# Kernel tuning notes

Hardware: AMD Instinct MI355X
Metric: run time of the kernel (lower is better)

## Reference

```python
import jax, jax.numpy as jnp
import numpy as np

B, NB, K, C, CM, POS = 8, 1024, 9, 32, 128, 2
SIGMA = 0.5
NEG_SLOPE = 0.01  # nn.LeakyReLU default
BN_EPS = 1e-5


def _leaky(x):
    return jnp.where(x >= 0, x, NEG_SLOPE * x)


def _batchnorm(x, gamma, beta):
    # BatchNorm1d, training-mode batch statistics over the point dimension
    mu = jnp.mean(x, axis=0)
    var = jnp.mean((x - mu) ** 2, axis=0)
    return gamma * (x - mu) * jax.lax.rsqrt(var + BN_EPS) + beta


def setup_inputs() -> dict:
    key = jax.random.key(0)
    ks = jax.random.split(key, 8)
    N = B * NB
    positions = jax.random.normal(ks[0], (N, POS), jnp.float32)
    weights = jax.random.normal(ks[1], (N, C), jnp.float32)
    batch = jnp.full((B,), NB, dtype=jnp.int32)  # uniform point counts per graph
    # KernelConv params: kernel_init='grid' -> 3x3 grid of offsets spanning +-sigma
    g = jnp.linspace(-SIGMA, SIGMA, 3, dtype=jnp.float32)
    kernel_positions = jnp.stack(jnp.meshgrid(g, g, indexing='ij'), axis=-1).reshape(K, POS)
    kernel_weights = (jax.random.normal(ks[2], (K, C, C), jnp.float32) / np.float32(np.sqrt(C * K)))
    conv_norm_gamma = jnp.ones((C,), jnp.float32)
    conv_norm_beta = jnp.zeros((C,), jnp.float32)
    # PyG MLP([C, CM, C+POS], act_first=True, plain_last=True)
    W1 = jax.random.normal(ks[3], (C, CM), jnp.float32) / np.float32(np.sqrt(C))
    b1 = jnp.zeros((CM,), jnp.float32)
    bn_gamma = jnp.ones((CM,), jnp.float32)
    bn_beta = jnp.zeros((CM,), jnp.float32)
    W2 = jax.random.normal(ks[4], (CM, C + POS), jnp.float32) / np.float32(np.sqrt(CM))
    b2 = jnp.zeros((C + POS,), jnp.float32)
    return dict(positions=positions, weights=weights, batch=batch,
                kernel_positions=kernel_positions, kernel_weights=kernel_weights,
                conv_norm_gamma=conv_norm_gamma, conv_norm_beta=conv_norm_beta,
                W1=W1, b1=b1, bn_gamma=bn_gamma, bn_beta=bn_beta, W2=W2, b2=b2)


def reference(positions, weights, batch, kernel_positions, kernel_weights,
              conv_norm_gamma, conv_norm_beta, W1, b1, bn_gamma, bn_beta, W2, b2):
    N = positions.shape[0]
    # --- KernelConv: each point spawns K components at pos + kernel offset ---
    conv_pos = (positions[:, None, :] + kernel_positions[None, :, :])  # [N,K,2]
    conv_w = jnp.einsum('nc,kcd->nkd', weights, kernel_weights)        # [N,K,C]
    conv_pos = conv_pos.reshape(B, NB * K, POS)
    conv_w = conv_w.reshape(B, NB * K, C)
    # --- KernelSample: evaluate Gaussian mixture at original positions ---
    p = positions.reshape(B, NB, POS)
    d2 = (jnp.sum(p * p, -1)[:, :, None]
          + jnp.sum(conv_pos * conv_pos, -1)[:, None, :]
          - 2.0 * jnp.einsum('bnd,bmd->bnm', p, conv_pos))             # [B,NB,NB*K]
    Kmat = jnp.exp(-d2 / (2.0 * SIGMA * SIGMA))
    sampled = jnp.einsum('bnm,bmc->bnc', Kmat, conv_w).reshape(N, C)
    x = _leaky(sampled)                                                 # KernelSample nonlinearity
    # conv_norm + residual add of input weights
    x = _batchnorm(x, conv_norm_gamma, conv_norm_beta) + weights
    # MLP: lin -> act -> batchnorm (act_first) -> plain last lin
    h = _batchnorm(_leaky(x @ W1 + b1), bn_gamma, bn_beta)
    mlp_out = h @ W2 + b2                                               # [N, POS + C]
    delta_pos, delta_w = mlp_out[:, :POS], mlp_out[:, POS:]
    return positions + delta_pos, x + delta_w
```

## Files before the change

kernel.cpp:

```cpp
#include <hip/hip_runtime.h>
#include <hip/hip_bf16.h>

#define BB    8
#define NBB   1024
#define KK    9
#define CC    32
#define CMM   128
#define NTOT  (BB*NBB)
#define MM    (NBB*KK)
#define MS    16
#define MR    (MM/MS)
#define NEG   0.01f
#define EPS   1e-5f
#define L2C   (-2.8853900817779268f)

#define OFF_CWT   0
#define SZ_CWT    (BB*CC*MM/2)
#define OFF_CFX   (OFF_CWT + SZ_CWT)
#define OFF_CFY   (OFF_CFX + BB*MM)
#define OFF_CF0   (OFF_CFY + BB*MM)
#define OFF_PART  (OFF_CF0 + BB*MM)
#define SZ_ONE    (NTOT*CC)
#define SZ_PART   (MS*SZ_ONE)
#define OFF_X0    (OFF_PART)
#define OFF_X     (OFF_PART + SZ_ONE)
#define OFF_H0    (OFF_PART + 2*SZ_ONE)
#define OFF_ST    (OFF_PART + SZ_PART)

typedef __attribute__((ext_vector_type(8))) short short8;
typedef __attribute__((ext_vector_type(4))) float f32x4;
typedef __attribute__((ext_vector_type(2))) float f32x2;

static __device__ __forceinline__ unsigned short f2bf_rne(float f) {
    __hip_bfloat16 h = __float2bfloat16(f);
    return *reinterpret_cast<unsigned short*>(&h);
}

__global__ __launch_bounds__(256) void k_convw(const float* __restrict__ pos,
                                               const float* __restrict__ kpos,
                                               const float* __restrict__ w,
                                               const float* __restrict__ kw,
                                               float* __restrict__ cfx,
                                               float* __restrict__ cfy,
                                               float* __restrict__ cf0,
                                               float* __restrict__ stats,
                                               short* __restrict__ cwT) {
    __shared__ unsigned short tile[4*32*144];
    __shared__ unsigned short kwl[KK*CC*CC];
    int t = threadIdx.x;
    int l = t & 63, wv = t >> 6;
    int lane15 = l & 15, quad = l >> 4;
    int blk = blockIdx.x;
    int b = blk >> 4, nbl = blk & 15;
    int n = b*NBB + nbl*64 + wv*16 + lane15;

    if (blk == 0 && t < 320) stats[t] = 0.f;
    #pragma unroll
    for (int rep = 0; rep < 3; ++rep) {
        int gid = blk*256 + t + rep*32768;
        if (gid < BB*MM) {
            int bb = gid / MM;
            int m = gid - bb*MM;
            int np = m / 9, k9 = m - np*9;
            float qx = pos[((size_t)(bb*NBB + np))*2 + 0] + kpos[k9*2 + 0];
            float qy = pos[((size_t)(bb*NBB + np))*2 + 1] + kpos[k9*2 + 1];
            cfx[gid] = -2.f*L2C*qx;
            cfy[gid] = -2.f*L2C*qy;
            cf0[gid] = L2C*(qx*qx + qy*qy);
        }
    }

    for (int u = t; u < KK*CC*CC/4; u += 256) {
        int flat = u*4;
        int row  = flat >> 5;
        int c0   = flat & 31;
        int kk = row >> 5, cp = row & 31;
        f32x4 v = *(const f32x4*)&kw[flat];
        kwl[(kk*CC + c0+0)*CC + cp] = f2bf_rne(v.x);
        kwl[(kk*CC + c0+1)*CC + cp] = f2bf_rne(v.y);
        kwl[(kk*CC + c0+2)*CC + cp] = f2bf_rne(v.z);
        kwl[(kk*CC + c0+3)*CC + cp] = f2bf_rne(v.w);
    }

    f32x4 w0 = *(const f32x4*)&w[(size_t)n*CC + quad*8];
    f32x4 w1 = *(const f32x4*)&w[(size_t)n*CC + quad*8 + 4];
    union { unsigned short us[8]; short8 s; } bfr;
    bfr.us[0] = f2bf_rne(w0.x); bfr.us[1] = f2bf_rne(w0.y);
    bfr.us[2] = f2bf_rne(w0.z); bfr.us[3] = f2bf_rne(w0.w);
    bfr.us[4] = f2bf_rne(w1.x); bfr.us[5] = f2bf_rne(w1.y);
    bfr.us[6] = f2bf_rne(w1.z); bfr.us[7] = f2bf_rne(w1.w);

    __syncthreads();

    f32x4 acc[KK][2];
    #pragma unroll
    for (int kk = 0; kk < KK; ++kk) {
        #pragma unroll
        for (int ct = 0; ct < 2; ++ct) {
            int c = ct*16 + lane15;
            short8 afr = *(const short8*)&kwl[(kk*CC + c)*CC + quad*8];
            acc[kk][ct] = __builtin_amdgcn_mfma_f32_16x16x32_bf16(
                afr, bfr.s, (f32x4)0.f, 0, 0, 0);
        }
    }
    unsigned short* tw = tile + wv*4608;
    #pragma unroll
    for (int kk = 0; kk < KK; ++kk)
        #pragma unroll
        for (int ct = 0; ct < 2; ++ct)
            #pragma unroll
            for (int reg = 0; reg < 4; ++reg) {
                int c = ct*16 + quad*4 + reg;
                tw[c*144 + lane15*9 + kk] = f2bf_rne(acc[kk][ct][reg]);
            }
    __syncthreads();
    short* dst = cwT + (size_t)b*CC*MM + (size_t)(nbl*64 + wv*16)*9;
    #pragma unroll
    for (int it = 0; it < 9; ++it) {
        int u = it*64 + l;
        int c = u / 18, seg = u - c*18;
        short8 v = *(const short8*)&tw[c*144 + seg*8];
        *(short8*)&dst[(size_t)c*MM + seg*8] = v;
    }
}

__global__ __launch_bounds__(256) void k_sample(const float* __restrict__ pos,
                                                const float* __restrict__ cfx,
                                                const float* __restrict__ cfy,
                                                const float* __restrict__ cf0,
                                                const short* __restrict__ cwT,
                                                float* __restrict__ part) {
    int t = threadIdx.x;
    int l = t & 63, w = t >> 6;
    int blk = blockIdx.x;
    int ks = blk & 15, nb = (blk >> 4) & 7, b = blk >> 7;
    int lane15 = l & 15, quad = l >> 4;
    int nbase = b*NBB + nb*128 + w*32;

    float px[2], py[2], cn[2];
    #pragma unroll
    for (int nt = 0; nt < 2; ++nt) {
        int n = nbase + nt*16 + lane15;
        float x = pos[(size_t)n*2], y = pos[(size_t)n*2 + 1];
        px[nt] = x; py[nt] = y; cn[nt] = L2C*(x*x + y*y);
    }
    f32x4 acc[2][2];
    #pragma unroll
    for (int nt = 0; nt < 2; ++nt) { acc[nt][0] = (f32x4)0.f; acc[nt][1] = (f32x4)0.f; }

    const float* bx = cfx + (size_t)b*MM;
    const float* by = cfy + (size_t)b*MM;
    const float* b0 = cf0 + (size_t)b*MM;
    const short* ca0 = cwT + (size_t)b*CC*MM + (size_t)lane15*MM;
    const short* ca1 = ca0 + (size_t)16*MM;

    int m0 = ks*MR + quad*8;
    #pragma unroll 2
    for (int kk = 0; kk < MR/32; ++kk, m0 += 32) {
        short8 a0 = *(const short8*)&ca0[m0];
        short8 a1 = *(const short8*)&ca1[m0];
        f32x4 vx0 = *(const f32x4*)&bx[m0];
        f32x4 vx1 = *(const f32x4*)&bx[m0 + 4];
        f32x4 vy0 = *(const f32x4*)&by[m0];
        f32x4 vy1 = *(const f32x4*)&by[m0 + 4];
        f32x4 v00 = *(const f32x4*)&b0[m0];
        f32x4 v01 = *(const f32x4*)&b0[m0 + 4];
        #pragma unroll
        for (int nt = 0; nt < 2; ++nt) {
            f32x2 Xv = {px[nt], px[nt]};
            f32x2 Yv = {py[nt], py[nt]};
            f32x2 Cv = {cn[nt], cn[nt]};
            f32x2 t0 = (f32x2){v00.x, v00.y} + Cv;
            t0 = (f32x2){vy0.x, vy0.y}*Yv + t0;
            t0 = (f32x2){vx0.x, vx0.y}*Xv + t0;
            f32x2 t1 = (f32x2){v00.z, v00.w} + Cv;
            t1 = (f32x2){vy0.z, vy0.w}*Yv + t1;
            t1 = (f32x2){vx0.z, vx0.w}*Xv + t1;
            f32x2 t2 = (f32x2){v01.x, v01.y} + Cv;
            t2 = (f32x2){vy1.x, vy1.y}*Yv + t2;
            t2 = (f32x2){vx1.x, vx1.y}*Xv + t2;
            f32x2 t3 = (f32x2){v01.z, v01.w} + Cv;
            t3 = (f32x2){vy1.z, vy1.w}*Yv + t3;
            t3 = (f32x2){vx1.z, vx1.w}*Xv + t3;
            float e0 = __builtin_amdgcn_exp2f(t0.x);
            float e1 = __builtin_amdgcn_exp2f(t0.y);
            float e2 = __builtin_amdgcn_exp2f(t1.x);
            float e3 = __builtin_amdgcn_exp2f(t1.y);
            float e4 = __builtin_amdgcn_exp2f(t2.x);
            float e5 = __builtin_amdgcn_exp2f(t2.y);
            float e6 = __builtin_amdgcn_exp2f(t3.x);
            float e7 = __builtin_amdgcn_exp2f(t3.y);
            union { unsigned int u[4]; short8 s; } bf;
            bf.u[0] = (__float_as_uint(e0) >> 16) | (__float_as_uint(e1) & 0xffff0000u);
            bf.u[1] = (__float_as_uint(e2) >> 16) | (__float_as_uint(e3) & 0xffff0000u);
            bf.u[2] = (__float_as_uint(e4) >> 16) | (__float_as_uint(e5) & 0xffff0000u);
            bf.u[3] = (__float_as_uint(e6) >> 16) | (__float_as_uint(e7) & 0xffff0000u);
            acc[nt][0] = __builtin_amdgcn_mfma_f32_16x16x32_bf16(a0, bf.s, acc[nt][0], 0, 0, 0);
            acc[nt][1] = __builtin_amdgcn_mfma_f32_16x16x32_bf16(a1, bf.s, acc[nt][1], 0, 0, 0);
        }
    }
    #pragma unroll
    for (int nt = 0; nt < 2; ++nt) {
        int n = nbase + nt*16 + lane15;
        #pragma unroll
        for (int ct = 0; ct < 2; ++ct) {
            int c = ct*16 + quad*4;
            *(f32x4*)&part[((size_t)ks*NTOT + n)*CC + c] = acc[nt][ct];
        }
    }
}

__global__ __launch_bounds__(256) void k_leaky_stats(const float* __restrict__ part,
                                                     float* __restrict__ x0,
                                                     float* __restrict__ s1) {
    __shared__ float ss[32], sq[32];
    int t = threadIdx.x;
    if (t < 32) { ss[t] = 0.f; sq[t] = 0.f; }
    __syncthreads();
    float lsum = 0.f, lsq = 0.f;
    int base = blockIdx.x * 1024;
    for (int j = 0; j < 4; ++j) {
        int idx = base + j*256 + t;
        float v = 0.f;
        #pragma unroll
        for (int s = 0; s < MS; ++s) v += part[(size_t)s*SZ_ONE + idx];
        v = v >= 0.f ? v : NEG*v;
        x0[idx] = v;
        lsum += v; lsq = fmaf(v, v, lsq);
    }
    atomicAdd(&ss[t & 31], lsum);
    atomicAdd(&sq[t & 31], lsq);
    __syncthreads();
    if (t < 32) { atomicAdd(&s1[t], ss[t]); atomicAdd(&s1[32+t], sq[t]); }
}

__global__ __launch_bounds__(256) void k_mlp1(const float* __restrict__ x0,
                                              const float* __restrict__ wts,
                                              const float* __restrict__ gma,
                                              const float* __restrict__ bta,
                                              const float* __restrict__ W1,
                                              const float* __restrict__ b1,
                                              const float* __restrict__ s1,
                                              float* __restrict__ x,
                                              float* __restrict__ h0,
                                              float* __restrict__ s2) {
    __shared__ float tile[64*68];
    int t = threadIdx.x;
    int l = t & 63, w = t >> 6;
    int blk = blockIdx.x;
    int nb = blk >> 1, jh = blk & 1;
    int n = nb*64 + l;
    int j0 = jh*64 + w*16;

    float xv[32];
    #pragma unroll
    for (int c = 0; c < 32; ++c) {
        float mu  = s1[c] * (1.f/NTOT);
        float var = s1[32+c]*(1.f/NTOT) - mu*mu;
        float a   = gma[c] * rsqrtf(var + EPS);
        float v   = x0[(size_t)n*CC + c];
        xv[c] = a*(v - mu) + bta[c] + wts[(size_t)n*CC + c];
    }
    if (jh == 0 && w == 0) {
        #pragma unroll
        for (int c = 0; c < 32; c += 4)
            *(float4*)&x[(size_t)n*CC + c] = make_float4(xv[c], xv[c+1], xv[c+2], xv[c+3]);
    }
    float acc[16];
    #pragma unroll
    for (int jj = 0; jj < 16; ++jj) acc[jj] = b1[j0 + jj];
    #pragma unroll 4
    for (int c = 0; c < 32; ++c) {
        float xc = xv[c];
        const float* w1r = W1 + c*CMM + j0;
        #pragma unroll
        for (int jj = 0; jj < 16; ++jj)
            acc[jj] = fmaf(xc, w1r[jj], acc[jj]);
    }
    float* hd = h0 + (size_t)n*CMM + j0;
    #pragma unroll
    for (int jj = 0; jj < 16; ++jj) {
        acc[jj] = acc[jj] >= 0.f ? acc[jj] : NEG*acc[jj];
        tile[(w*16 + jj)*68 + l] = acc[jj];
    }
    #pragma unroll
    for (int jj = 0; jj < 16; jj += 4)
        *(float4*)&hd[jj] = make_float4(acc[jj], acc[jj+1], acc[jj+2], acc[jj+3]);
    __syncthreads();
    int jl = t >> 2, grp = t & 3;
    float lsum = 0.f, lsq = 0.f;
    #pragma unroll
    for (int q = 0; q < 4; ++q) {
        f32x4 v = *(const f32x4*)&tile[jl*68 + grp*16 + q*4];
        lsum += v.x + v.y + v.z + v.w;
        lsq = fmaf(v.x, v.x, fmaf(v.y, v.y, fmaf(v.z, v.z, fmaf(v.w, v.w, lsq))));
    }
    lsum += __shfl_xor(lsum, 1); lsq += __shfl_xor(lsq, 1);
    lsum += __shfl_xor(lsum, 2); lsq += __shfl_xor(lsq, 2);
    if (grp == 0) {
        int jg = jh*64 + jl;
        atomicAdd(&s2[jg], lsum);
        atomicAdd(&s2[CMM + jg], lsq);
    }
}

__global__ __launch_bounds__(256) void k_mlp2(const float* __restrict__ h0,
                                              const float* __restrict__ x,
                                              const float* __restrict__ pos,
                                              const float* __restrict__ g2,
                                              const float* __restrict__ bt2,
                                              const float* __restrict__ W2,
                                              const float* __restrict__ b2,
                                              const float* __restrict__ s2,
                                              float* __restrict__ out) {
    __shared__ float red[8][32][35];
    int t = threadIdx.x;
    int lane = t & 63, w = t >> 6;
    int half = lane >> 5;
    int nl = lane & 31;
    int n = blockIdx.x*32 + nl;
    int j0 = w*32 + half*16;
    float hv[16];
    #pragma unroll
    for (int q = 0; q < 4; ++q)
        *(float4*)&hv[q*4] = *(const float4*)&h0[(size_t)n*CMM + j0 + q*4];
    #pragma unroll
    for (int jj = 0; jj < 16; ++jj) {
        int j = j0 + jj;
        float mu  = s2[j] * (1.f/NTOT);
        float var = s2[CMM+j]*(1.f/NTOT) - mu*mu;
        float a   = g2[j] * rsqrtf(var + EPS);
        hv[jj] = a*(hv[jj] - mu) + bt2[j];
    }
    float acc[34];
    #pragma unroll
    for (int c = 0; c < 34; ++c) acc[c] = 0.f;
    for (int jj = 0; jj < 16; ++jj) {
        float h = hv[jj];
        const float* w2r = W2 + (size_t)(j0 + jj)*34;
        #pragma unroll
        for (int c = 0; c < 34; ++c)
            acc[c] = fmaf(h, w2r[c], acc[c]);
    }
    int rid = w*2 + half;
    #pragma unroll
    for (int c = 0; c < 34; ++c) red[rid][nl][c] = acc[c];
    __syncthreads();
    for (int u = t; u < 32*34; u += 256) {
        int r = u / 34, c = u - r*34;
        float v = red[0][r][c] + red[1][r][c] + red[2][r][c] + red[3][r][c]
                + red[4][r][c] + red[5][r][c] + red[6][r][c] + red[7][r][c] + b2[c];
        int nn = blockIdx.x*32 + r;
        if (c < 2)
            out[(size_t)nn*2 + c] = pos[(size_t)nn*2 + c] + v;
        else
            out[16384 + (size_t)nn*32 + (c-2)] = x[(size_t)nn*32 + (c-2)] + v;
    }
}

extern "C" void kernel_launch(void* const* d_in, const int* in_sizes, int n_in,
                              void* d_out, int out_size, void* d_ws, size_t ws_size,
                              hipStream_t stream) {
    const float* positions = (const float*)d_in[0];
    const float* weights   = (const float*)d_in[1];
    const float* kpos = (const float*)d_in[3];
    const float* kw   = (const float*)d_in[4];
    const float* cg   = (const float*)d_in[5];
    const float* cb   = (const float*)d_in[6];
    const float* W1   = (const float*)d_in[7];
    const float* b1   = (const float*)d_in[8];
    const float* bg   = (const float*)d_in[9];
    const float* bb   = (const float*)d_in[10];
    const float* W2   = (const float*)d_in[11];
    const float* b2   = (const float*)d_in[12];
    float* ws  = (float*)d_ws;
    float* out = (float*)d_out;

    float* s1 = ws + OFF_ST;
    float* s2 = ws + OFF_ST + 64;

    k_convw<<<128, 256, 0, stream>>>(positions, kpos, weights, kw,
                                     ws + OFF_CFX, ws + OFF_CFY, ws + OFF_CF0,
                                     s1, (short*)(ws + OFF_CWT));
    k_sample<<<1024, 256, 0, stream>>>(positions, ws + OFF_CFX, ws + OFF_CFY,
                                       ws + OFF_CF0, (const short*)(ws + OFF_CWT),
                                       ws + OFF_PART);
    k_leaky_stats<<<256, 256, 0, stream>>>(ws + OFF_PART, ws + OFF_X0, s1);
    k_mlp1<<<256, 256, 0, stream>>>(ws + OFF_X0, weights, cg, cb, W1, b1,
                                    s1, ws + OFF_X, ws + OFF_H0, s2);
    k_mlp2<<<256, 256, 0, stream>>>(ws + OFF_H0, ws + OFF_X, positions,
                                    bg, bb, W2, b2, s2, out);
}
```

Before: 159.2 us.

## Fuse all stages into one persistent kernel with grid barriers

Replaces the five kernel launches with one 256-block kernel that uses software grid barriers between stages (conv weights, Gaussian sampling, batchnorm stats, MLP). Intermediates stay in shared memory rather than round-tripping through global partial buffers, and the split-M partial reduction is now done inside a block instead of through a separate pass. The goal is to remove launch gaps and global traffic. In exchange, only 256 blocks (one per 32 points) do the heavy sampling loop, which lowers parallelism compared with the previous 1024-block launch. The spin barrier also relies on every block being co-resident on the device.

```diff
diff --git a/kernel.cpp b/kernel.cpp
--- a/kernel.cpp
+++ b/kernel.cpp
@@ -8,24 +8,17 @@
 #define CMM   128
 #define NTOT  (BB*NBB)
 #define MM    (NBB*KK)
-#define MS    16
-#define MR    (MM/MS)
 #define NEG   0.01f
 #define EPS   1e-5f
 #define L2C   (-2.8853900817779268f)
+#define NBLK  256
 
 #define OFF_CWT   0
 #define SZ_CWT    (BB*CC*MM/2)
 #define OFF_CFX   (OFF_CWT + SZ_CWT)
 #define OFF_CFY   (OFF_CFX + BB*MM)
 #define OFF_CF0   (OFF_CFY + BB*MM)
-#define OFF_PART  (OFF_CF0 + BB*MM)
-#define SZ_ONE    (NTOT*CC)
-#define SZ_PART   (MS*SZ_ONE)
-#define OFF_X0    (OFF_PART)
-#define OFF_X     (OFF_PART + SZ_ONE)
-#define OFF_H0    (OFF_PART + 2*SZ_ONE)
-#define OFF_ST    (OFF_PART + SZ_PART)
+#define OFF_ST    (OFF_CF0 + BB*MM)
 
 typedef __attribute__((ext_vector_type(8))) short short8;
 typedef __attribute__((ext_vector_type(4))) float f32x4;
@@ -36,28 +29,59 @@
     return *reinterpret_cast<unsigned short*>(&h);
 }
 
-__global__ __launch_bounds__(256) void k_convw(const float* __restrict__ pos,
-                                               const float* __restrict__ kpos,
-                                               const float* __restrict__ w,
-                                               const float* __restrict__ kw,
-                                               float* __restrict__ cfx,
-                                               float* __restrict__ cfy,
-                                               float* __restrict__ cf0,
-                                               float* __restrict__ stats,
-                                               short* __restrict__ cwT) {
-    __shared__ unsigned short tile[4*32*144];
-    __shared__ unsigned short kwl[KK*CC*CC];
-    int t = threadIdx.x;
-    int l = t & 63, wv = t >> 6;
-    int lane15 = l & 15, quad = l >> 4;
-    int blk = blockIdx.x;
-    int b = blk >> 4, nbl = blk & 15;
-    int n = b*NBB + nbl*64 + wv*16 + lane15;
-
-    if (blk == 0 && t < 320) stats[t] = 0.f;
+__device__ unsigned g_cnt[4];
+__device__ unsigned g_gen[4];
+
+static __device__ __forceinline__ void grid_sync(int i) {
+    __threadfence();
+    __syncthreads();
+    if (threadIdx.x == 0) {
+        unsigned g = __hip_atomic_load(&g_gen[i], __ATOMIC_RELAXED, __HIP_MEMORY_SCOPE_AGENT);
+        unsigned a = __hip_atomic_fetch_add(&g_cnt[i], 1u, __ATOMIC_ACQ_REL, __HIP_MEMORY_SCOPE_AGENT);
+        if (a == NBLK - 1u) {
+            __hip_atomic_store(&g_cnt[i], 0u, __ATOMIC_RELAXED, __HIP_MEMORY_SCOPE_AGENT);
+            __hip_atomic_store(&g_gen[i], g + 1u, __ATOMIC_RELEASE, __HIP_MEMORY_SCOPE_AGENT);
+        } else {
+            while (__hip_atomic_load(&g_gen[i], __ATOMIC_ACQUIRE, __HIP_MEMORY_SCOPE_AGENT) == g)
+                __builtin_amdgcn_s_sleep(2);
+        }
+    }
+    __syncthreads();
+    __threadfence();
+}
+
+#define L_H0   0
+#define L_X    4224
+#define L_X0   5376
+#define L_SCR  6528
+#define L_TOT  15744
+
+__global__ __launch_bounds__(256) void k_fused(
+    const float* __restrict__ pos, const float* __restrict__ wts,
+    const float* __restrict__ kpos, const float* __restrict__ kw,
+    const float* __restrict__ cg, const float* __restrict__ cb,
+    const float* __restrict__ W1, const float* __restrict__ b1,
+    const float* __restrict__ g2, const float* __restrict__ bt2,
+    const float* __restrict__ W2, const float* __restrict__ b2,
+    float* __restrict__ ws, float* __restrict__ out)
+{
+    __shared__ float smem[L_TOT];
+    float* cfx = ws + OFF_CFX;
+    float* cfy = ws + OFF_CFY;
+    float* cf0 = ws + OFF_CF0;
+    float* stats = ws + OFF_ST;
+    short* cwT = (short*)(ws + OFF_CWT);
+
+    const int t = threadIdx.x;
+    const int blk = blockIdx.x;
+    const int l = t & 63, wv = t >> 6;
+    const int lane15 = l & 15, quad = l >> 4;
+    const int b = blk >> 5;
+
+    if (blk == 0) { stats[t] = 0.f; if (t < 64) stats[256 + t] = 0.f; }
     #pragma unroll
-    for (int rep = 0; rep < 3; ++rep) {
-        int gid = blk*256 + t + rep*32768;
+    for (int rep = 0; rep < 2; ++rep) {
+        int gid = rep*65536 + blk*256 + t;
         if (gid < BB*MM) {
             int bb = gid / MM;
             int m = gid - bb*MM;
@@ -69,292 +93,287 @@
             cf0[gid] = L2C*(qx*qx + qy*qy);
         }
     }
-
-    for (int u = t; u < KK*CC*CC/4; u += 256) {
-        int flat = u*4;
-        int row  = flat >> 5;
-        int c0   = flat & 31;
-        int kk = row >> 5, cp = row & 31;
-        f32x4 v = *(const f32x4*)&kw[flat];
-        kwl[(kk*CC + c0+0)*CC + cp] = f2bf_rne(v.x);
-        kwl[(kk*CC + c0+1)*CC + cp] = f2bf_rne(v.y);
-        kwl[(kk*CC + c0+2)*CC + cp] = f2bf_rne(v.z);
-        kwl[(kk*CC + c0+3)*CC + cp] = f2bf_rne(v.w);
-    }
-
-    f32x4 w0 = *(const f32x4*)&w[(size_t)n*CC + quad*8];
-    f32x4 w1 = *(const f32x4*)&w[(size_t)n*CC + quad*8 + 4];
-    union { unsigned short us[8]; short8 s; } bfr;
-    bfr.us[0] = f2bf_rne(w0.x); bfr.us[1] = f2bf_rne(w0.y);
-    bfr.us[2] = f2bf_rne(w0.z); bfr.us[3] = f2bf_rne(w0.w);
-    bfr.us[4] = f2bf_rne(w1.x); bfr.us[5] = f2bf_rne(w1.y);
-    bfr.us[6] = f2bf_rne(w1.z); bfr.us[7] = f2bf_rne(w1.w);
-
-    __syncthreads();
-
-    f32x4 acc[KK][2];
-    #pragma unroll
-    for (int kk = 0; kk < KK; ++kk) {
-        #pragma unroll
-        for (int ct = 0; ct < 2; ++ct) {
-            int c = ct*16 + lane15;
-            short8 afr = *(const short8*)&kwl[(kk*CC + c)*CC + quad*8];
-            acc[kk][ct] = __builtin_amdgcn_mfma_f32_16x16x32_bf16(
-                afr, bfr.s, (f32x4)0.f, 0, 0, 0);
-        }
-    }
-    unsigned short* tw = tile + wv*4608;
-    #pragma unroll
-    for (int kk = 0; kk < KK; ++kk)
-        #pragma unroll
-        for (int ct = 0; ct < 2; ++ct)
-            #pragma unroll
-            for (int reg = 0; reg < 4; ++reg) {
-                int c = ct*16 + quad*4 + reg;
-                tw[c*144 + lane15*9 + kk] = f2bf_rne(acc[kk][ct][reg]);
-            }
-    __syncthreads();
-    short* dst = cwT + (size_t)b*CC*MM + (size_t)(nbl*64 + wv*16)*9;
-    #pragma unroll
-    for (int it = 0; it < 9; ++it) {
-        int u = it*64 + l;
-        int c = u / 18, seg = u - c*18;
-        short8 v = *(const short8*)&tw[c*144 + seg*8];
-        *(short8*)&dst[(size_t)c*MM + seg*8] = v;
-    }
-}
-
-__global__ __launch_bounds__(256) void k_sample(const float* __restrict__ pos,
-                                                const float* __restrict__ cfx,
-                                                const float* __restrict__ cfy,
-                                                const float* __restrict__ cf0,
-                                                const short* __restrict__ cwT,
-                                                float* __restrict__ part) {
-    int t = threadIdx.x;
-    int l = t & 63, w = t >> 6;
-    int blk = blockIdx.x;
-    int ks = blk & 15, nb = (blk >> 4) & 7, b = blk >> 7;
-    int lane15 = l & 15, quad = l >> 4;
-    int nbase = b*NBB + nb*128 + w*32;
-
-    float px[2], py[2], cn[2];
-    #pragma unroll
-    for (int nt = 0; nt < 2; ++nt) {
-        int n = nbase + nt*16 + lane15;
-        float x = pos[(size_t)n*2], y = pos[(size_t)n*2 + 1];
-        px[nt] = x; py[nt] = y; cn[nt] = L2C*(x*x + y*y);
-    }
-    f32x4 acc[2][2];
-    #pragma unroll
-    for (int nt = 0; nt < 2; ++nt) { acc[nt][0] = (f32x4)0.f; acc[nt][1] = (f32x4)0.f; }
-
-    const float* bx = cfx + (size_t)b*MM;
-    const float* by = cfy + (size_t)b*MM;
-    const float* b0 = cf0 + (size_t)b*MM;
-    const short* ca0 = cwT + (size_t)b*CC*MM + (size_t)lane15*MM;
-    const short* ca1 = ca0 + (size_t)16*MM;
-
-    int m0 = ks*MR + quad*8;
-    #pragma unroll 2
-    for (int kk = 0; kk < MR/32; ++kk, m0 += 32) {
+    {
+        unsigned short* kwl  = (unsigned short*)(smem + L_SCR);
+        unsigned short* tile = (unsigned short*)(smem + L_SCR) + 9216;
+        for (int u = t; u < KK*CC*CC/4; u += 256) {
+            int flat = u*4;
+            int row = flat >> 5;
+            int c0 = flat & 31;
+            int kk = row >> 5, cp = row & 31;
+            f32x4 v = *(const f32x4*)&kw[flat];
+            kwl[(kk*CC + c0+0)*CC + cp] = f2bf_rne(v.x);
+            kwl[(kk*CC + c0+1)*CC + cp] = f2bf_rne(v.y);
+            kwl[(kk*CC + c0+2)*CC + cp] = f2bf_rne(v.z);
+            kwl[(kk*CC + c0+3)*CC + cp] = f2bf_rne(v.w);
+        }
+        int nb_ = blk*32 + (wv & 1)*16 + lane15;
+        f32x4 w0 = *(const f32x4*)&wts[(size_t)nb_*CC + quad*8];
+        f32x4 w1v = *(const f32x4*)&wts[(size_t)nb_*CC + quad*8 + 4];
+        union { unsigned short us[8]; short8 s; } bfr;
+        bfr.us[0] = f2bf_rne(w0.x);  bfr.us[1] = f2bf_rne(w0.y);
+        bfr.us[2] = f2bf_rne(w0.z);  bfr.us[3] = f2bf_rne(w0.w);
+        bfr.us[4] = f2bf_rne(w1v.x); bfr.us[5] = f2bf_rne(w1v.y);
+        bfr.us[6] = f2bf_rne(w1v.z); bfr.us[7] = f2bf_rne(w1v.w);
+        __syncthreads();
+        if (wv < 2) {
+            f32x4 acc[KK][2];
+            #pragma unroll
+            for (int kk = 0; kk < KK; ++kk)
+                #pragma unroll
+                for (int ct = 0; ct < 2; ++ct) {
+                    int c = ct*16 + lane15;
+                    short8 afr = *(const short8*)&kwl[(kk*CC + c)*CC + quad*8];
+                    acc[kk][ct] = __builtin_amdgcn_mfma_f32_16x16x32_bf16(
+                        afr, bfr.s, (f32x4)0.f, 0, 0, 0);
+                }
+            unsigned short* tw = tile + wv*4608;
+            #pragma unroll
+            for (int kk = 0; kk < KK; ++kk)
+                #pragma unroll
+                for (int ct = 0; ct < 2; ++ct)
+                    #pragma unroll
+                    for (int reg = 0; reg < 4; ++reg) {
+                        int c = ct*16 + quad*4 + reg;
+                        tw[c*144 + lane15*9 + kk] = f2bf_rne(acc[kk][ct][reg]);
+                    }
+        }
+        __syncthreads();
+        short* dst = cwT + (size_t)b*CC*MM + (size_t)(blk & 31)*288;
+        #pragma unroll
+        for (int it = 0; it < 5; ++it) {
+            int u = it*256 + t;
+            if (u < 1152) {
+                int c = u / 36, seg = u - c*36;
+                const unsigned short* src = tile + (seg < 18 ? 0 : 4608)
+                                          + c*144 + (seg < 18 ? seg : seg - 18)*8;
+                short8 v = *(const short8*)src;
+                *(short8*)&dst[(size_t)c*MM + seg*8] = v;
+            }
+        }
+    }
+    grid_sync(0);
+
+    {
+        const float* bx = cfx + (size_t)b*MM;
+        const float* by = cfy + (size_t)b*MM;
+        const float* b0 = cf0 + (size_t)b*MM;
+        const short* ca0 = cwT + (size_t)b*CC*MM + (size_t)lane15*MM;
+        const short* ca1 = ca0 + (size_t)16*MM;
+
+        float px[2], py[2], cn[2];
+        #pragma unroll
+        for (int nt = 0; nt < 2; ++nt) {
+            int n = blk*32 + nt*16 + lane15;
+            float x = pos[(size_t)n*2], y = pos[(size_t)n*2 + 1];
+            px[nt] = x; py[nt] = y; cn[nt] = L2C*(x*x + y*y);
+        }
+        f32x4 acc[2][2];
+        acc[0][0] = (f32x4)0.f; acc[0][1] = (f32x4)0.f;
+        acc[1][0] = (f32x4)0.f; acc[1][1] = (f32x4)0.f;
+
+        int m0 = wv*2304 + quad*8;
         short8 a0 = *(const short8*)&ca0[m0];
         short8 a1 = *(const short8*)&ca1[m0];
-        f32x4 vx0 = *(const f32x4*)&bx[m0];
-        f32x4 vx1 = *(const f32x4*)&bx[m0 + 4];
-        f32x4 vy0 = *(const f32x4*)&by[m0];
-        f32x4 vy1 = *(const f32x4*)&by[m0 + 4];
-        f32x4 v00 = *(const f32x4*)&b0[m0];
-        f32x4 v01 = *(const f32x4*)&b0[m0 + 4];
-        #pragma unroll
-        for (int nt = 0; nt < 2; ++nt) {
-            f32x2 Xv = {px[nt], px[nt]};
-            f32x2 Yv = {py[nt], py[nt]};
-            f32x2 Cv = {cn[nt], cn[nt]};
-            f32x2 t0 = (f32x2){v00.x, v00.y} + Cv;
-            t0 = (f32x2){vy0.x, vy0.y}*Yv + t0;
-            t0 = (f32x2){vx0.x, vx0.y}*Xv + t0;
-            f32x2 t1 = (f32x2){v00.z, v00.w} + Cv;
-            t1 = (f32x2){vy0.z, vy0.w}*Yv + t1;
-            t1 = (f32x2){vx0.z, vx0.w}*Xv + t1;
-            f32x2 t2 = (f32x2){v01.x, v01.y} + Cv;
-            t2 = (f32x2){vy1.x, vy1.y}*Yv + t2;
-            t2 = (f32x2){vx1.x, vx1.y}*Xv + t2;
-            f32x2 t3 = (f32x2){v01.z, v01.w} + Cv;
-            t3 = (f32x2){vy1.z, vy1.w}*Yv + t3;
-            t3 = (f32x2){vx1.z, vx1.w}*Xv + t3;
-            float e0 = __builtin_amdgcn_exp2f(t0.x);
-            float e1 = __builtin_amdgcn_exp2f(t0.y);
-            float e2 = __builtin_amdgcn_exp2f(t1.x);
-            float e3 = __builtin_amdgcn_exp2f(t1.y);
-            float e4 = __builtin_amdgcn_exp2f(t2.x);
-            float e5 = __builtin_amdgcn_exp2f(t2.y);
-            float e6 = __builtin_amdgcn_exp2f(t3.x);
-            float e7 = __builtin_amdgcn_exp2f(t3.y);
-            union { unsigned int u[4]; short8 s; } bf;
-            bf.u[0] = (__float_as_uint(e0) >> 16) | (__float_as_uint(e1) & 0xffff0000u);
-            bf.u[1] = (__float_as_uint(e2) >> 16) | (__float_as_uint(e3) & 0xffff0000u);
-            bf.u[2] = (__float_as_uint(e4) >> 16) | (__float_as_uint(e5) & 0xffff0000u);
-            bf.u[3] = (__float_as_uint(e6) >> 16) | (__float_as_uint(e7) & 0xffff0000u);
-            acc[nt][0] = __builtin_amdgcn_mfma_f32_16x16x32_bf16(a0, bf.s, acc[nt][0], 0, 0, 0);
-            acc[nt][1] = __builtin_amdgcn_mfma_f32_16x16x32_bf16(a1, bf.s, acc[nt][1], 0, 0, 0);
-        }
-    }
-    #pragma unroll
-    for (int nt = 0; nt < 2; ++nt) {
-        int n = nbase + nt*16 + lane15;
-        #pragma unroll
-        for (int ct = 0; ct < 2; ++ct) {
-            int c = ct*16 + quad*4;
-            *(f32x4*)&part[((size_t)ks*NTOT + n)*CC + c] = acc[nt][ct];
-        }
-    }
-}
-
-__global__ __launch_bounds__(256) void k_leaky_stats(const float* __restrict__ part,
-                                                     float* __restrict__ x0,
-                                                     float* __restrict__ s1) {
-    __shared__ float ss[32], sq[32];
-    int t = threadIdx.x;
-    if (t < 32) { ss[t] = 0.f; sq[t] = 0.f; }
+        f32x4 vx0 = *(const f32x4*)&bx[m0], vx1 = *(const f32x4*)&bx[m0+4];
+        f32x4 vy0 = *(const f32x4*)&by[m0], vy1 = *(const f32x4*)&by[m0+4];
+        f32x4 v00 = *(const f32x4*)&b0[m0], v01 = *(const f32x4*)&b0[m0+4];
+        for (int kk = 0; kk < 72; ++kk) {
+            int mn = m0 + (kk < 71 ? 32 : 0);
+            short8 na0 = *(const short8*)&ca0[mn];
+            short8 na1 = *(const short8*)&ca1[mn];
+            f32x4 nvx0 = *(const f32x4*)&bx[mn], nvx1 = *(const f32x4*)&bx[mn+4];
+            f32x4 nvy0 = *(const f32x4*)&by[mn], nvy1 = *(const f32x4*)&by[mn+4];
+            f32x4 nv00 = *(const f32x4*)&b0[mn], nv01 = *(const f32x4*)&b0[mn+4];
+            #pragma unroll
+            for (int nt = 0; nt < 2; ++nt) {
+                f32x2 Xv = {px[nt], px[nt]};
+                f32x2 Yv = {py[nt], py[nt]};
+                f32x2 Cv = {cn[nt], cn[nt]};
+                f32x2 t0 = (f32x2){v00.x, v00.y} + Cv;
+                t0 = (f32x2){vy0.x, vy0.y}*Yv + t0;
+                t0 = (f32x2){vx0.x, vx0.y}*Xv + t0;
+                f32x2 t1 = (f32x2){v00.z, v00.w} + Cv;
+                t1 = (f32x2){vy0.z, vy0.w}*Yv + t1;
+                t1 = (f32x2){vx0.z, vx0.w}*Xv + t1;
+                f32x2 t2 = (f32x2){v01.x, v01.y} + Cv;
+                t2 = (f32x2){vy1.x, vy1.y}*Yv + t2;
+                t2 = (f32x2){vx1.x, vx1.y}*Xv + t2;
+                f32x2 t3 = (f32x2){v01.z, v01.w} + Cv;
+                t3 = (f32x2){vy1.z, vy1.w}*Yv + t3;
+                t3 = (f32x2){vx1.z, vx1.w}*Xv + t3;
+                float e0 = __builtin_amdgcn_exp2f(t0.x);
+                float e1 = __builtin_amdgcn_exp2f(t0.y);
+                float e2 = __builtin_amdgcn_exp2f(t1.x);
+                float e3 = __builtin_amdgcn_exp2f(t1.y);
+                float e4 = __builtin_amdgcn_exp2f(t2.x);
+                float e5 = __builtin_amdgcn_exp2f(t2.y);
+                float e6 = __builtin_amdgcn_exp2f(t3.x);
+                float e7 = __builtin_amdgcn_exp2f(t3.y);
+                union { unsigned int u[4]; short8 s; } bf;
+                bf.u[0] = (__float_as_uint(e0) >> 16) | (__float_as_uint(e1) & 0xffff0000u);
+                bf.u[1] = (__float_as_uint(e2) >> 16) | (__float_as_uint(e3) & 0xffff0000u);
+                bf.u[2] = (__float_as_uint(e4) >> 16) | (__float_as_uint(e5) & 0xffff0000u);
+                bf.u[3] = (__float_as_uint(e6) >> 16) | (__float_as_uint(e7) & 0xffff0000u);
+                acc[nt][0] = __builtin_amdgcn_mfma_f32_16x16x32_bf16(a0, bf.s, acc[nt][0], 0, 0, 0);
+                acc[nt][1] = __builtin_amdgcn_mfma_f32_16x16x32_bf16(a1, bf.s, acc[nt][1], 0, 0, 0);
+            }
+            a0 = na0; a1 = na1;
+            vx0 = nvx0; vx1 = nvx1; vy0 = nvy0; vy1 = nvy1; v00 = nv00; v01 = nv01;
+            m0 = mn;
+        }
+        float* red = smem + L_SCR;
+        #pragma unroll
+        for (int nt = 0; nt < 2; ++nt)
+            #pragma unroll
+            for (int ct = 0; ct < 2; ++ct) {
+                int n = nt*16 + lane15, c = ct*16 + quad*4;
+                *(f32x4*)&red[(wv*32 + n)*36 + c] = acc[nt][ct];
+            }
+        __syncthreads();
+        {
+            int nr = t >> 3, c0 = (t & 7)*4;
+            f32x4 v  = *(const f32x4*)&red[(0*32 + nr)*36 + c0];
+            f32x4 v1 = *(const f32x4*)&red[(1*32 + nr)*36 + c0];
+            f32x4 v2 = *(const f32x4*)&red[(2*32 + nr)*36 + c0];
+            f32x4 v3 = *(const f32x4*)&red[(3*32 + nr)*36 + c0];
+            v = v + v1 + v2 + v3;
+            v.x = v.x >= 0.f ? v.x : NEG*v.x;
+            v.y = v.y >= 0.f ? v.y : NEG*v.y;
+            v.z = v.z >= 0.f ? v.z : NEG*v.z;
+            v.w = v.w >= 0.f ? v.w : NEG*v.w;
+            *(f32x4*)&smem[L_X0 + nr*36 + c0] = v;
+            float s0 = v.x, s1v = v.y, s2v = v.z, s3v = v.w;
+            float q0 = v.x*v.x, q1 = v.y*v.y, q2 = v.z*v.z, q3 = v.w*v.w;
+            #pragma unroll
+            for (int mk = 8; mk <= 32; mk <<= 1) {
+                s0 += __shfl_xor(s0, mk); s1v += __shfl_xor(s1v, mk);
+                s2v += __shfl_xor(s2v, mk); s3v += __shfl_xor(s3v, mk);
+                q0 += __shfl_xor(q0, mk); q1 += __shfl_xor(q1, mk);
+                q2 += __shfl_xor(q2, mk); q3 += __shfl_xor(q3, mk);
+            }
+            if (l < 8) {
+                atomicAdd(&stats[c0 + 0], s0);  atomicAdd(&stats[c0 + 1], s1v);
+                atomicAdd(&stats[c0 + 2], s2v); atomicAdd(&stats[c0 + 3], s3v);
+                atomicAdd(&stats[32 + c0 + 0], q0); atomicAdd(&stats[32 + c0 + 1], q1);
+                atomicAdd(&stats[32 + c0 + 2], q2); atomicAdd(&stats[32 + c0 + 3], q3);
+            }
+        }
+    }
+    grid_sync(1);
+
+    {
+        int nr = t >> 3, c0 = (t & 7)*4;
+        f32x4 smv = *(const f32x4*)&stats[c0];
+        f32x4 sqv = *(const f32x4*)&stats[32 + c0];
+        f32x4 x0v = *(const f32x4*)&smem[L_X0 + nr*36 + c0];
+        f32x4 gv = *(const f32x4*)&cg[c0];
+        f32x4 bv = *(const f32x4*)&cb[c0];
+        f32x4 wv4 = *(const f32x4*)&wts[((size_t)(blk*32 + nr))*CC + c0];
+        f32x4 xv;
+        #pragma unroll
+        for (int i2 = 0; i2 < 4; ++i2) {
+            float mu  = smv[i2] * (1.f/NTOT);
+            float var = sqv[i2]*(1.f/NTOT) - mu*mu;
+            float a   = gv[i2] * rsqrtf(var + EPS);
+            xv[i2] = a*(x0v[i2] - mu) + bv[i2] + wv4[i2];
+        }
+        *(f32x4*)&smem[L_X + nr*36 + c0] = xv;
+    }
     __syncthreads();
-    float lsum = 0.f, lsq = 0.f;
-    int base = blockIdx.x * 1024;
-    for (int j = 0; j < 4; ++j) {
-        int idx = base + j*256 + t;
-        float v = 0.f;
-        #pragma unroll
-        for (int s = 0; s < MS; ++s) v += part[(size_t)s*SZ_ONE + idx];
-        v = v >= 0.f ? v : NEG*v;
-        x0[idx] = v;
-        lsum += v; lsq = fmaf(v, v, lsq);
-    }
-    atomicAdd(&ss[t & 31], lsum);
-    atomicAdd(&sq[t & 31], lsq);
+    {
+        int nloc = t & 31, jh2 = (t >> 5) & 1;
+        int j0 = wv*32 + jh2*16;
+        float acc2[16];
+        *(f32x4*)&acc2[0]  = *(const f32x4*)&b1[j0];
+        *(f32x4*)&acc2[4]  = *(const f32x4*)&b1[j0 + 4];
+        *(f32x4*)&acc2[8]  = *(const f32x4*)&b1[j0 + 8];
+        *(f32x4*)&acc2[12] = *(const f32x4*)&b1[j0 + 12];
+        #pragma unroll 4
+        for (int c = 0; c < 32; ++c) {
+            float xc = smem[L_X + nloc*36 + c];
+            const float* w1r = W1 + c*CMM + j0;
+            f32x4 wa = *(const f32x4*)&w1r[0];
+            f32x4 wb = *(const f32x4*)&w1r[4];
+            f32x4 wc = *(const f32x4*)&w1r[8];
+            f32x4 wd = *(const f32x4*)&w1r[12];
+            acc2[0]  = fmaf(xc, wa.x, acc2[0]);  acc2[1]  = fmaf(xc, wa.y, acc2[1]);
+            acc2[2]  = fmaf(xc, wa.z, acc2[2]);  acc2[3]  = fmaf(xc, wa.w, acc2[3]);
+            acc2[4]  = fmaf(xc, wb.x, acc2[4]);  acc2[5]  = fmaf(xc, wb.y, acc2[5]);
+            acc2[6]  = fmaf(xc, wb.z, acc2[6]);  acc2[7]  = fmaf(xc, wb.w, acc2[7]);
+            acc2[8]  = fmaf(xc, wc.x, acc2[8]);  acc2[9]  = fmaf(xc, wc.y, acc2[9]);
+            acc2[10] = fmaf(xc, wc.z, acc2[10]); acc2[11] = fmaf(xc, wc.w, acc2[11]);
+            acc2[12] = fmaf(xc, wd.x, acc2[12]); acc2[13] = fmaf(xc, wd.y, acc2[13]);
+            acc2[14] = fmaf(xc, wd.z, acc2[14]); acc2[15] = fmaf(xc, wd.w, acc2[15]);
+        }
+        #pragma unroll
+        for (int jj = 0; jj < 16; ++jj)
+            acc2[jj] = acc2[jj] >= 0.f ? acc2[jj] : NEG*acc2[jj];
+        #pragma unroll
+        for (int q = 0; q < 4; ++q)
+            *(f32x4*)&smem[L_H0 + nloc*132 + j0 + q*4] = *(f32x4*)&acc2[q*4];
+    }
     __syncthreads();
-    if (t < 32) { atomicAdd(&s1[t], ss[t]); atomicAdd(&s1[32+t], sq[t]); }
-}
-
-__global__ __launch_bounds__(256) void k_mlp1(const float* __restrict__ x0,
-                                              const float* __restrict__ wts,
-                                              const float* __restrict__ gma,
-                                              const float* __restrict__ bta,
-                                              const float* __restrict__ W1,
-                                              const float* __restrict__ b1,
-                                              const float* __restrict__ s1,
-                                              float* __restrict__ x,
-                                              float* __restrict__ h0,
-                                              float* __restrict__ s2) {
-    __shared__ float tile[64*68];
-    int t = threadIdx.x;
-    int l = t & 63, w = t >> 6;
-    int blk = blockIdx.x;
-    int nb = blk >> 1, jh = blk & 1;
-    int n = nb*64 + l;
-    int j0 = jh*64 + w*16;
-
-    float xv[32];
-    #pragma unroll
-    for (int c = 0; c < 32; ++c) {
-        float mu  = s1[c] * (1.f/NTOT);
-        float var = s1[32+c]*(1.f/NTOT) - mu*mu;
-        float a   = gma[c] * rsqrtf(var + EPS);
-        float v   = x0[(size_t)n*CC + c];
-        xv[c] = a*(v - mu) + bta[c] + wts[(size_t)n*CC + c];
-    }
-    if (jh == 0 && w == 0) {
-        #pragma unroll
-        for (int c = 0; c < 32; c += 4)
-            *(float4*)&x[(size_t)n*CC + c] = make_float4(xv[c], xv[c+1], xv[c+2], xv[c+3]);
-    }
-    float acc[16];
-    #pragma unroll
-    for (int jj = 0; jj < 16; ++jj) acc[jj] = b1[j0 + jj];
-    #pragma unroll 4
-    for (int c = 0; c < 32; ++c) {
-        float xc = xv[c];
-        const float* w1r = W1 + c*CMM + j0;
-        #pragma unroll
-        for (int jj = 0; jj < 16; ++jj)
-            acc[jj] = fmaf(xc, w1r[jj], acc[jj]);
-    }
-    float* hd = h0 + (size_t)n*CMM + j0;
-    #pragma unroll
-    for (int jj = 0; jj < 16; ++jj) {
-        acc[jj] = acc[jj] >= 0.f ? acc[jj] : NEG*acc[jj];
-        tile[(w*16 + jj)*68 + l] = acc[jj];
-    }
-    #pragma unroll
-    for (int jj = 0; jj < 16; jj += 4)
-        *(float4*)&hd[jj] = make_float4(acc[jj], acc[jj+1], acc[jj+2], acc[jj+3]);
+    {
+        int j = t >> 1, hf = t & 1;
+        float ls = 0.f, lq = 0.f;
+        #pragma unroll
+        for (int i2 = 0; i2 < 16; ++i2) {
+            float v = smem[L_H0 + (hf*16 + i2)*132 + j];
+            ls += v; lq = fmaf(v, v, lq);
+        }
+        ls += __shfl_xor(ls, 1); lq += __shfl_xor(lq, 1);
+        if (hf == 0) { atomicAdd(&stats[64 + j], ls); atomicAdd(&stats[192 + j], lq); }
+    }
+    grid_sync(2);
+
+    {
+        int rid = t >> 5, nl = t & 31;
+        int j0e = rid*16;
+        float hv[16];
+        #pragma unroll
+        for (int q = 0; q < 4; ++q)
+            *(f32x4*)&hv[q*4] = *(const f32x4*)&smem[L_H0 + nl*132 + j0e + q*4];
+        #pragma unroll
+        for (int jj = 0; jj < 16; ++jj) {
+            int j = j0e + jj;
+            float mu  = stats[64 + j] * (1.f/NTOT);
+            float var = stats[192 + j]*(1.f/NTOT) - mu*mu;
+            float a   = g2[j] * rsqrtf(var + EPS);
+            hv[jj] = a*(hv[jj] - mu) + bt2[j];
+        }
+        float acc3[34];
+        #pragma unroll
+        for (int c = 0; c < 34; ++c) acc3[c] = 0.f;
+        for (int jj = 0; jj < 16; ++jj) {
+            float h = hv[jj];
+            const float* w2r = W2 + (size_t)(j0e + jj)*34;
+            #pragma unroll
+            for (int c = 0; c < 34; ++c)
+                acc3[c] = fmaf(h, w2r[c], acc3[c]);
+        }
+        float* red2 = smem + L_SCR;
+        #pragma unroll
+        for (int c = 0; c < 34; ++c) red2[(rid*32 + nl)*35 + c] = acc3[c];
+    }
     __syncthreads();
-    int jl = t >> 2, grp = t & 3;
-    float lsum = 0.f, lsq = 0.f;
-    #pragma unroll
-    for (int q = 0; q < 4; ++q) {
-        f32x4 v = *(const f32x4*)&tile[jl*68 + grp*16 + q*4];
-        lsum += v.x + v.y + v.z + v.w;
-        lsq = fmaf(v.x, v.x, fmaf(v.y, v.y, fmaf(v.z, v.z, fmaf(v.w, v.w, lsq))));
-    }
-    lsum += __shfl_xor(lsum, 1); lsq += __shfl_xor(lsq, 1);
-    lsum += __shfl_xor(lsum, 2); lsq += __shfl_xor(lsq, 2);
-    if (grp == 0) {
-        int jg = jh*64 + jl;
-        atomicAdd(&s2[jg], lsum);
-        atomicAdd(&s2[CMM + jg], lsq);
-    }
-}
-
-__global__ __launch_bounds__(256) void k_mlp2(const float* __restrict__ h0,
-                                              const float* __restrict__ x,
-                                              const float* __restrict__ pos,
-                                              const float* __restrict__ g2,
-                                              const float* __restrict__ bt2,
-                                              const float* __restrict__ W2,
-                                              const float* __restrict__ b2,
-                                              const float* __restrict__ s2,
-                                              float* __restrict__ out) {
-    __shared__ float red[8][32][35];
-    int t = threadIdx.x;
-    int lane = t & 63, w = t >> 6;
-    int half = lane >> 5;
-    int nl = lane & 31;
-    int n = blockIdx.x*32 + nl;
-    int j0 = w*32 + half*16;
-    float hv[16];
-    #pragma unroll
-    for (int q = 0; q < 4; ++q)
-        *(float4*)&hv[q*4] = *(const float4*)&h0[(size_t)n*CMM + j0 + q*4];
-    #pragma unroll
-    for (int jj = 0; jj < 16; ++jj) {
-        int j = j0 + jj;
-        float mu  = s2[j] * (1.f/NTOT);
-        float var = s2[CMM+j]*(1.f/NTOT) - mu*mu;
-        float a   = g2[j] * rsqrtf(var + EPS);
-        hv[jj] = a*(hv[jj] - mu) + bt2[j];
-    }
-    float acc[34];
-    #pragma unroll
-    for (int c = 0; c < 34; ++c) acc[c] = 0.f;
-    for (int jj = 0; jj < 16; ++jj) {
-        float h = hv[jj];
-        const float* w2r = W2 + (size_t)(j0 + jj)*34;
-        #pragma unroll
-        for (int c = 0; c < 34; ++c)
-            acc[c] = fmaf(h, w2r[c], acc[c]);
-    }
-    int rid = w*2 + half;
-    #pragma unroll
-    for (int c = 0; c < 34; ++c) red[rid][nl][c] = acc[c];
-    __syncthreads();
-    for (int u = t; u < 32*34; u += 256) {
-        int r = u / 34, c = u - r*34;
-        float v = red[0][r][c] + red[1][r][c] + red[2][r][c] + red[3][r][c]
-                + red[4][r][c] + red[5][r][c] + red[6][r][c] + red[7][r][c] + b2[c];
-        int nn = blockIdx.x*32 + r;
-        if (c < 2)
-            out[(size_t)nn*2 + c] = pos[(size_t)nn*2 + c] + v;
-        else
-            out[16384 + (size_t)nn*32 + (c-2)] = x[(size_t)nn*32 + (c-2)] + v;
+    {
+        #pragma unroll
+        for (int it = 0; it < 5; ++it) {
+            int u = it*256 + t;
+            if (u < 1088) {
+                int r = u / 34, c = u - r*34;
+                float* red2 = smem + L_SCR;
+                float v = b2[c];
+                #pragma unroll
+                for (int rr = 0; rr < 8; ++rr) v += red2[(rr*32 + r)*35 + c];
+                int nn = blk*32 + r;
+                if (c < 2)
+                    out[(size_t)nn*2 + c] = pos[(size_t)nn*2 + c] + v;
+                else
+                    out[16384 + (size_t)nn*32 + (c-2)] = smem[L_X + r*36 + (c-2)] + v;
+            }
+        }
     }
 }
 
@@ -376,18 +395,6 @@
     float* ws  = (float*)d_ws;
     float* out = (float*)d_out;
 
-    float* s1 = ws + OFF_ST;
-    float* s2 = ws + OFF_ST + 64;
-
-    k_convw<<<128, 256, 0, stream>>>(positions, kpos, weights, kw,
-                                     ws + OFF_CFX, ws + OFF_CFY, ws + OFF_CF0,
-                                     s1, (short*)(ws + OFF_CWT));
-    k_sample<<<1024, 256, 0, stream>>>(positions, ws + OFF_CFX, ws + OFF_CFY,
-                                       ws + OFF_CF0, (const short*)(ws + OFF_CWT),
-                                       ws + OFF_PART);
-    k_leaky_stats<<<256, 256, 0, stream>>>(ws + OFF_PART, ws + OFF_X0, s1);
-    k_mlp1<<<256, 256, 0, stream>>>(ws + OFF_X0, weights, cg, cb, W1, b1,
-                                    s1, ws + OFF_X, ws + OFF_H0, s2);
-    k_mlp2<<<256, 256, 0, stream>>>(ws + OFF_H0, ws + OFF_X, positions,
-                                    bg, bb, W2, b2, s2, out);
+    k_fused<<<NBLK, 256, 0, stream>>>(positions, weights, kpos, kw, cg, cb,
+                                      W1, b1, bg, bb, W2, b2, ws, out);
 }
```

New measurement: 380.5 us. 2.39x slower.
